# Kernel tuning notes

Measured on AMD Instinct MI355X. Metric: run time of the kernel, lower is better.

Reference implementation:

```python
import jax, jax.numpy as jnp
import numpy as np

OUT = 7   # output_size
SR = 2    # sampling_ratio


def _roi_align(feat, boxes, out_size, sr):
    """torchvision-style ROIAlign, spatial_scale=1.0, aligned=False.
    feat: [N,C,H,W], boxes: [K,5] (batch_idx,x1,y1,x2,y2) -> [K,C,out,out]."""
    N, C, H, W = feat.shape
    b = boxes[:, 0].astype(jnp.int32)                      # [K]
    x1, y1, x2, y2 = boxes[:, 1], boxes[:, 2], boxes[:, 3], boxes[:, 4]
    roi_w = jnp.maximum(x2 - x1, 1.0)
    roi_h = jnp.maximum(y2 - y1, 1.0)
    bin_h = roi_h / out_size
    bin_w = roi_w / out_size
    # sample offsets within each bin: (i + 0.5)/sr, i in [0,sr)
    off = (jnp.arange(sr, dtype=feat.dtype) + 0.5) / sr    # [sr]
    p = jnp.arange(out_size, dtype=feat.dtype)             # [out]
    # ys: [K, out*sr], xs: [K, out*sr]
    ys = (y1[:, None, None] + (p[None, :, None] + off[None, None, :]) * bin_h[:, None, None]).reshape(-1, out_size * sr)
    xs = (x1[:, None, None] + (p[None, :, None] + off[None, None, :]) * bin_w[:, None, None]).reshape(-1, out_size * sr)
    K = ys.shape[0]
    S = out_size * sr
    y = jnp.broadcast_to(ys[:, :, None], (K, S, S)).reshape(K, S * S)  # [K,P]
    x = jnp.broadcast_to(xs[:, None, :], (K, S, S)).reshape(K, S * S)
    valid = (y >= -1.0) & (y <= H) & (x >= -1.0) & (x <= W)
    y = jnp.clip(y, 0.0, H - 1)
    x = jnp.clip(x, 0.0, W - 1)
    y_lo = jnp.floor(y).astype(jnp.int32)
    x_lo = jnp.floor(x).astype(jnp.int32)
    y_hi = jnp.minimum(y_lo + 1, H - 1)
    x_hi = jnp.minimum(x_lo + 1, W - 1)
    ly = y - y_lo.astype(y.dtype)
    lx = x - x_lo.astype(x.dtype)
    hy = 1.0 - ly
    hx = 1.0 - lx
    feat_flat = feat.reshape(N, C, H * W)
    bb = b[:, None, None]                                   # [K,1,1]
    cc = jnp.arange(C)[None, :, None]                       # [1,C,1]

    def gather(yi, xi):
        idx = (yi * W + xi)[:, None, :]                     # [K,1,P]
        return feat_flat[bb, cc, idx]                       # [K,C,P]

    v = (gather(y_lo, x_lo) * (hy * hx)[:, None, :]
         + gather(y_lo, x_hi) * (hy * lx)[:, None, :]
         + gather(y_hi, x_lo) * (ly * hx)[:, None, :]
         + gather(y_hi, x_hi) * (ly * lx)[:, None, :])
    v = jnp.where(valid[:, None, :], v, 0.0)
    # average the sr*sr samples per bin
    v = v.reshape(K, C, out_size, sr, out_size, sr).mean(axis=(3, 5))
    return v


def setup_inputs() -> dict:
    key = jax.random.key(0)
    k1, k2, k3, k4, k5, k6 = jax.random.split(key, 6)
    N, C, H, W = 4, 256, 200, 200
    K = 512
    Hb = H // 2  # boxes live in the half-height band coord frame
    features = jax.random.normal(k1, (N, C, H, W), dtype=jnp.float32)
    b = jax.random.randint(k2, (K,), 0, N).astype(jnp.float32)
    cx = jax.random.uniform(k3, (K,)) * W
    cy = jax.random.uniform(k4, (K,)) * Hb
    bw = jax.random.uniform(k5, (K,)) * 60.0 + 8.0
    bh = jax.random.uniform(k6, (K,)) * 40.0 + 8.0
    x1 = jnp.clip(cx - bw / 2, 0.0, W - 2.0)
    x2 = jnp.clip(cx + bw / 2, x1 + 1.0, float(W))
    y1 = jnp.clip(cy - bh / 2, 0.0, Hb - 2.0)
    y2 = jnp.clip(cy + bh / 2, y1 + 1.0, float(Hb))
    boxes = jnp.stack([b, x1, y1, x2, y2], axis=1).astype(jnp.float32)
    return {"features": features, "boxes": boxes}


def reference(features, boxes):
    H = features.shape[2]
    feat_b1 = features[:, :, : H // 2, :]
    feat_b2 = features[:, :, H // 2 :, :]
    out_b1 = _roi_align(feat_b1, boxes, OUT, SR)
    out_b2 = _roi_align(feat_b2, boxes, OUT, SR)
    return jnp.concatenate([out_b1, out_b2], axis=1)  # [K, 2C, OUT, OUT]
```

## Files before the change

kernel.cpp:

```cpp
#include <hip/hip_runtime.h>

#define OUTSZ 7
#define SR 2
#define SS (OUTSZ*SR)
#define NS (SS*SS)
#define C_BAND 256
#define H_BAND 100
#define W_FULL 200
#define PLANE (2*H_BAND*W_FULL)
#define CCHUNK 64
#define NCHUNK (C_BAND/CCHUNK)
#define NBOX 512

__global__ __launch_bounds__(256) void sort_boxes_kernel(
    const float* __restrict__ boxes, int* __restrict__ perm)
{
    __shared__ int keys[NBOX];
    __shared__ int vals[NBOX];
    const int tid = threadIdx.x;
    for (int i = tid; i < NBOX; i += 256) {
        const int n = (int)boxes[i*5 + 0];
        const int y = (int)boxes[i*5 + 2];
        keys[i] = n * 256 + y;
        vals[i] = i;
    }
    __syncthreads();
    for (int size = 2; size <= NBOX; size <<= 1) {
        for (int stride = size >> 1; stride > 0; stride >>= 1) {
            const int i = (tid / stride) * (stride * 2) + (tid % stride);
            const int j = i + stride;
            const bool up = ((i & size) == 0);
            const int ki = keys[i], kj = keys[j];
            if ((ki > kj) == up) {
                keys[i] = kj; keys[j] = ki;
                const int v = vals[i]; vals[i] = vals[j]; vals[j] = v;
            }
            __syncthreads();
        }
    }
    for (int i = tid; i < NBOX; i += 256) perm[i] = vals[i];
}

__global__ __launch_bounds__(256) void roi_align_kernel(
    const float* __restrict__ feat,
    const float* __restrict__ boxes,
    const int*   __restrict__ perm,
    float* __restrict__ out)
{
    __shared__ int    s_i0[NS];
    __shared__ int    s_i1[NS];
    __shared__ float4 s_w[NS];

    const int b     = blockIdx.x;
    const int j     = b & 7;
    const int chunk = j & 3;
    const int band  = j >> 2;
    const int k     = perm[b >> 3];

    const int tid = threadIdx.x;

    const float bxf = boxes[k*5 + 0];
    const float x1  = boxes[k*5 + 1];
    const float y1  = boxes[k*5 + 2];
    const float x2  = boxes[k*5 + 3];
    const float y2  = boxes[k*5 + 4];
    const int   n   = (int)bxf;

    const float roi_w = fmaxf(x2 - x1, 1.0f);
    const float roi_h = fmaxf(y2 - y1, 1.0f);
    const float bin_w = roi_w / 7.0f;
    const float bin_h = roi_h / 7.0f;

    if (tid < NS) {
        const int sy = tid / SS;
        const int sx = tid - sy * SS;
        const int ph = sy >> 1, iy = sy & 1;
        const int pw = sx >> 1, ix = sx & 1;
        float y = y1 + ((float)ph + ((float)iy + 0.5f) * 0.5f) * bin_h;
        float x = x1 + ((float)pw + ((float)ix + 0.5f) * 0.5f) * bin_w;
        const bool valid = (y >= -1.0f) && (y <= (float)H_BAND) &&
                           (x >= -1.0f) && (x <= (float)W_FULL);
        y = fminf(fmaxf(y, 0.0f), (float)(H_BAND - 1));
        x = fminf(fmaxf(x, 0.0f), (float)(W_FULL - 1));
        const int y_lo = (int)floorf(y);
        const int x_lo = (int)floorf(x);
        const int y_hi = min(y_lo + 1, H_BAND - 1);
        const float ly = y - (float)y_lo;
        const float lx = x - (float)x_lo;
        const float hy = 1.0f - ly, hx = 1.0f - lx;
        const int xb = min(x_lo, W_FULL - 2);
        float w0, w1;
        if (x_lo == xb) { w0 = hx; w1 = lx; }
        else            { w0 = 0.0f; w1 = hx + lx; }
        const float vs = valid ? 1.0f : 0.0f;
        s_i0[tid] = y_lo * W_FULL + xb;
        s_i1[tid] = y_hi * W_FULL + xb;
        s_w[tid] = make_float4(hy * w0 * vs, hy * w1 * vs,
                               ly * w0 * vs, ly * w1 * vs);
    }
    __syncthreads();

    const int c0 = chunk * CCHUNK;
    const float* fbase = feat + (size_t)(n * C_BAND + c0) * PLANE
                              + (size_t)band * (H_BAND * W_FULL);
    float* obase = out + ((size_t)k * (2*C_BAND) + (size_t)band * C_BAND + c0)
                       * (OUTSZ * OUTSZ);

    const int NOUT = CCHUNK * OUTSZ * OUTSZ;
    for (int o = tid; o < NOUT; o += 256) {
        const int c   = o / 49;
        const int bin = o - c * 49;
        const int ph  = bin / 7;
        const int pw  = bin - ph * 7;
        const float* fc = fbase + (size_t)c * PLANE;
        const int s00 = (ph * 2) * SS + pw * 2;
        float acc = 0.0f;
        #pragma unroll
        for (int iy = 0; iy < 2; ++iy) {
            #pragma unroll
            for (int ix = 0; ix < 2; ++ix) {
                const int s = s00 + iy * SS + ix;
                const float4 w = s_w[s];
                const float2 a = *(const float2*)(fc + s_i0[s]);
                const float2 d = *(const float2*)(fc + s_i1[s]);
                acc += w.x * a.x + w.y * a.y + w.z * d.x + w.w * d.y;
            }
        }
        obase[o] = acc * 0.25f;
    }
}

extern "C" void kernel_launch(void* const* d_in, const int* in_sizes, int n_in,
                              void* d_out, int out_size, void* d_ws, size_t ws_size,
                              hipStream_t stream) {
    const float* feat  = (const float*)d_in[0];
    const float* boxes = (const float*)d_in[1];
    float* out = (float*)d_out;
    int* perm = (int*)d_ws;

    sort_boxes_kernel<<<1, 256, 0, stream>>>(boxes, perm);
    const int nblocks = NBOX * 2 * NCHUNK;
    roi_align_kernel<<<nblocks, 256, 0, stream>>>(feat, boxes, perm, out);
}
```

Baseline: 325.3 us.

## Stage ROI feature patches into LDS via global_load_lds before bilinear sampling

Instead of each thread gathering float2 pairs straight from global memory, each wavefront copies the ROI's bounding row/column patch for one channel into LDS with global_load_lds, and 196 threads then do the bilinear interpolation from LDS. Channels are processed four at a time per iteration, with two block barriers each time. The aim is coalesced patch loads and less redundant global gather traffic. In exchange it adds many barriers, leaves most threads idle during compute, holds up to 31 offsets per thread in registers, and needs large LDS, which may cut occupancy. It also loads the entire patch even when samples are sparse.

Result: slower. 332.7 us (+2.3%).

```diff
diff --git a/kernel.cpp b/kernel.cpp
--- a/kernel.cpp
+++ b/kernel.cpp
@@ -1,16 +1,22 @@
 #include <hip/hip_runtime.h>
 
 #define OUTSZ 7
-#define SR 2
-#define SS (OUTSZ*SR)
-#define NS (SS*SS)
+#define SS 14
+#define NS 196
 #define C_BAND 256
 #define H_BAND 100
 #define W_FULL 200
 #define PLANE (2*H_BAND*W_FULL)
 #define CCHUNK 64
-#define NCHUNK (C_BAND/CCHUNK)
 #define NBOX 512
+#define NC 4
+#define MAXROWS 28
+#define MAXSPANP 69
+#define PATCHF (MAXROWS*MAXSPANP)
+#define MAXI 31
+
+typedef const __attribute__((address_space(1))) void gvoid_t;
+typedef __attribute__((address_space(3))) void lvoid_t;
 
 __global__ __launch_bounds__(256) void sort_boxes_kernel(
     const float* __restrict__ boxes, int* __restrict__ perm)
@@ -47,17 +53,18 @@
     const int*   __restrict__ perm,
     float* __restrict__ out)
 {
-    __shared__ int    s_i0[NS];
-    __shared__ int    s_i1[NS];
+    __shared__ float  patch[NC][PATCHF];
     __shared__ float4 s_w[NS];
+    __shared__ int    s_o0[NS];
+    __shared__ int    s_o1[NS];
+    __shared__ int    rowy[MAXROWS];
 
     const int b     = blockIdx.x;
-    const int j     = b & 7;
-    const int chunk = j & 3;
-    const int band  = j >> 2;
+    const int jj    = b & 7;
+    const int chunk = jj & 3;
+    const int band  = jj >> 2;
     const int k     = perm[b >> 3];
-
-    const int tid = threadIdx.x;
+    const int tid   = threadIdx.x;
 
     const float bxf = boxes[k*5 + 0];
     const float x1  = boxes[k*5 + 1];
@@ -71,62 +78,118 @@
     const float bin_w = roi_w / 7.0f;
     const float bin_h = roi_h / 7.0f;
 
+    const float xA = fminf(fmaxf(x1 + 0.25f*bin_w, 0.f), 199.f);
+    const float xB = fminf(fmaxf(x1 + 6.75f*bin_w, 0.f), 199.f);
+    const int xoff  = min((int)floorf(xA), W_FULL - 2);
+    const int xbmax = min((int)floorf(xB), W_FULL - 2);
+    const int spanw  = xbmax - xoff + 2;
+    const int spanwP = spanw | 1;
+    const float yA = fminf(fmaxf(y1 + 0.25f*bin_h, 0.f), 99.f);
+    const float yB = fminf(fmaxf(y1 + 6.75f*bin_h, 0.f), 99.f);
+    const int rmin   = (int)floorf(yA);
+    const int rmaxr  = min((int)floorf(yB) + 1, H_BAND - 1);
+    const int contig = rmaxr - rmin + 1;
+    const bool layoutA = (contig <= MAXROWS);
+    const int nr = layoutA ? contig : MAXROWS;
+
     if (tid < NS) {
         const int sy = tid / SS;
         const int sx = tid - sy * SS;
-        const int ph = sy >> 1, iy = sy & 1;
-        const int pw = sx >> 1, ix = sx & 1;
-        float y = y1 + ((float)ph + ((float)iy + 0.5f) * 0.5f) * bin_h;
-        float x = x1 + ((float)pw + ((float)ix + 0.5f) * 0.5f) * bin_w;
-        const bool valid = (y >= -1.0f) && (y <= (float)H_BAND) &&
-                           (x >= -1.0f) && (x <= (float)W_FULL);
-        y = fminf(fmaxf(y, 0.0f), (float)(H_BAND - 1));
-        x = fminf(fmaxf(x, 0.0f), (float)(W_FULL - 1));
+        float y = y1 + ((float)(sy>>1) + ((float)(sy&1) + 0.5f) * 0.5f) * bin_h;
+        float x = x1 + ((float)(sx>>1) + ((float)(sx&1) + 0.5f) * 0.5f) * bin_w;
+        const bool valid = (y >= -1.0f) && (y <= 100.0f) &&
+                           (x >= -1.0f) && (x <= 200.0f);
+        y = fminf(fmaxf(y, 0.f), 99.f);
+        x = fminf(fmaxf(x, 0.f), 199.f);
         const int y_lo = (int)floorf(y);
         const int x_lo = (int)floorf(x);
         const int y_hi = min(y_lo + 1, H_BAND - 1);
         const float ly = y - (float)y_lo;
         const float lx = x - (float)x_lo;
-        const float hy = 1.0f - ly, hx = 1.0f - lx;
+        const float hy = 1.f - ly, hx = 1.f - lx;
         const int xb = min(x_lo, W_FULL - 2);
         float w0, w1;
-        if (x_lo == xb) { w0 = hx; w1 = lx; }
-        else            { w0 = 0.0f; w1 = hx + lx; }
-        const float vs = valid ? 1.0f : 0.0f;
-        s_i0[tid] = y_lo * W_FULL + xb;
-        s_i1[tid] = y_hi * W_FULL + xb;
-        s_w[tid] = make_float4(hy * w0 * vs, hy * w1 * vs,
-                               ly * w0 * vs, ly * w1 * vs);
-    }
+        if (x_lo == xb) { w0 = hx;  w1 = lx; }
+        else            { w0 = 0.f; w1 = hx + lx; }
+        const float vs = valid ? 1.f : 0.f;
+        const int xr = xb - xoff;
+        int rs0, rs1;
+        if (layoutA) { rs0 = y_lo - rmin; rs1 = y_hi - rmin; }
+        else         { rs0 = 2*sy;        rs1 = 2*sy + 1;    }
+        s_o0[tid] = rs0 * spanwP + xr;
+        s_o1[tid] = rs1 * spanwP + xr;
+        s_w[tid] = make_float4(hy*w0*vs, hy*w1*vs, ly*w0*vs, ly*w1*vs);
+        if (!layoutA && sx == 0) { rowy[2*sy] = y_lo; rowy[2*sy + 1] = y_hi; }
+    }
+    if (layoutA && tid < nr) rowy[tid] = rmin + tid;
     __syncthreads();
 
+    const int lane = tid & 63;
+    const int wv   = tid >> 6;
+    const int M  = nr * spanwP;
+    const int nI = (M + 63) >> 6;
+    int goff[MAXI];
+    #pragma unroll
+    for (int i = 0; i < MAXI; ++i) {
+        goff[i] = -1;
+        if (i < nI) {
+            const int slot = lane + (i << 6);
+            if (slot < M) {
+                const int r  = slot / spanwP;
+                const int xq = slot - r * spanwP;
+                if (xq < spanw)
+                    goff[i] = (rowy[r] * W_FULL + xoff + xq) * 4;
+            }
+        }
+    }
+
     const int c0 = chunk * CCHUNK;
-    const float* fbase = feat + (size_t)(n * C_BAND + c0) * PLANE
-                              + (size_t)band * (H_BAND * W_FULL);
-    float* obase = out + ((size_t)k * (2*C_BAND) + (size_t)band * C_BAND + c0)
-                       * (OUTSZ * OUTSZ);
-
-    const int NOUT = CCHUNK * OUTSZ * OUTSZ;
-    for (int o = tid; o < NOUT; o += 256) {
-        const int c   = o / 49;
-        const int bin = o - c * 49;
-        const int ph  = bin / 7;
-        const int pw  = bin - ph * 7;
-        const float* fc = fbase + (size_t)c * PLANE;
-        const int s00 = (ph * 2) * SS + pw * 2;
-        float acc = 0.0f;
+    const char* fb = (const char*)(feat + (size_t)(n * C_BAND + c0) * PLANE
+                                        + (size_t)band * (H_BAND * W_FULL));
+    float* ob = out + ((size_t)k * (2*C_BAND) + (size_t)band * C_BAND + c0)
+                    * (OUTSZ * OUTSZ);
+
+    const size_t cstride = (size_t)PLANE * 4;
+    const char* cb = fb + (size_t)wv * cstride;
+
+    for (int it = 0; it < CCHUNK / NC; ++it) {
         #pragma unroll
-        for (int iy = 0; iy < 2; ++iy) {
+        for (int i = 0; i < MAXI; ++i) {
+            if (i < nI) {
+                if (goff[i] >= 0) {
+                    __builtin_amdgcn_global_load_lds(
+                        (gvoid_t*)(cb + goff[i]),
+                        (lvoid_t*)(&patch[wv][i << 6]),
+                        4, 0, 0);
+                }
+            }
+        }
+        __syncthreads();
+
+        if (tid < NS) {
+            const int c_sub = tid / 49;
+            const int bin   = tid - c_sub * 49;
+            const int ph = bin / 7;
+            const int pw = bin - ph * 7;
+            const float* pb = &patch[c_sub][0];
+            const int s00 = (ph * 2) * SS + pw * 2;
+            float acc = 0.f;
             #pragma unroll
-            for (int ix = 0; ix < 2; ++ix) {
-                const int s = s00 + iy * SS + ix;
-                const float4 w = s_w[s];
-                const float2 a = *(const float2*)(fc + s_i0[s]);
-                const float2 d = *(const float2*)(fc + s_i1[s]);
-                acc += w.x * a.x + w.y * a.y + w.z * d.x + w.w * d.y;
-            }
-        }
-        obase[o] = acc * 0.25f;
+            for (int iy = 0; iy < 2; ++iy) {
+                #pragma unroll
+                for (int ix = 0; ix < 2; ++ix) {
+                    const int s = s00 + iy * SS + ix;
+                    const float4 w = s_w[s];
+                    const int o0 = s_o0[s];
+                    const int o1 = s_o1[s];
+                    acc += w.x * pb[o0] + w.y * pb[o0 + 1]
+                         + w.z * pb[o1] + w.w * pb[o1 + 1];
+                }
+            }
+            ob[(it * NC + c_sub) * 49 + bin] = acc * 0.25f;
+        }
+        __syncthreads();
+        cb += (size_t)NC * cstride;
     }
 }
 
@@ -139,6 +202,6 @@
     int* perm = (int*)d_ws;
 
     sort_boxes_kernel<<<1, 256, 0, stream>>>(boxes, perm);
-    const int nblocks = NBOX * 2 * NCHUNK;
+    const int nblocks = NBOX * 2 * 4;
     roi_align_kernel<<<nblocks, 256, 0, stream>>>(feat, boxes, perm, out);
 }
```

## Transpose features to channels-last and gather ROI samples with coalesced channel loads

Applied to the files above, without the earlier changes.

Adds a transpose kernel that writes the feature map to NHWC in workspace, then a gather kernel where each lane handles one channel, so every bilinear tap is a coalesced load across channels. Blocks are remapped so that units sharing an XCD process neighbouring sorted boxes, and results are staged through shared memory so the NCHW output is written coalesced. The cost is a full transpose of the whole 164MB feature map on every call, plus a larger workspace; a fallback to the old kernel remains for when the workspace is too small.

Result: slower. 358.2 us (+10.1%).

```diff
diff --git a/kernel.cpp b/kernel.cpp
--- a/kernel.cpp
+++ b/kernel.cpp
@@ -1,16 +1,15 @@
 #include <hip/hip_runtime.h>
 
 #define OUTSZ 7
-#define SR 2
-#define SS (OUTSZ*SR)
-#define NS (SS*SS)
+#define SS 14
+#define NS 196
 #define C_BAND 256
 #define H_BAND 100
+#define H_FULL 200
 #define W_FULL 200
-#define PLANE (2*H_BAND*W_FULL)
-#define CCHUNK 64
-#define NCHUNK (C_BAND/CCHUNK)
+#define POS (H_FULL*W_FULL)
 #define NBOX 512
+#define FEATT_OFF 4096
 
 __global__ __launch_bounds__(256) void sort_boxes_kernel(
     const float* __restrict__ boxes, int* __restrict__ perm)
@@ -41,23 +40,68 @@
     for (int i = tid; i < NBOX; i += 256) perm[i] = vals[i];
 }
 
-__global__ __launch_bounds__(256) void roi_align_kernel(
-    const float* __restrict__ feat,
+__global__ __launch_bounds__(256) void transpose_kernel(
+    const float* __restrict__ feat, float* __restrict__ featT)
+{
+    __shared__ float tile[64][65];
+    const int b    = blockIdx.x;
+    const int pt   = b % 625;
+    const int cg   = (b / 625) & 3;
+    const int n    = b / 2500;
+    const int c0   = cg * 64;
+    const int pos0 = pt * 64;
+    const int tid  = threadIdx.x;
+
+    {
+        const int xq = tid & 15;
+        const int cb = tid >> 4;
+        const float* src = feat + (size_t)(n * C_BAND + c0) * POS + pos0;
+        #pragma unroll
+        for (int r = 0; r < 4; ++r) {
+            const int ci = cb + (r << 4);
+            const float4 v = *(const float4*)(src + (size_t)ci * POS + (xq << 2));
+            tile[ci][(xq<<2)+0] = v.x;
+            tile[ci][(xq<<2)+1] = v.y;
+            tile[ci][(xq<<2)+2] = v.z;
+            tile[ci][(xq<<2)+3] = v.w;
+        }
+    }
+    __syncthreads();
+    {
+        const int cq = tid & 15;
+        const int pb = tid >> 4;
+        float* dst = featT + ((size_t)n * POS + pos0) * C_BAND + c0;
+        #pragma unroll
+        for (int r = 0; r < 4; ++r) {
+            const int pi = pb + (r << 4);
+            float4 v;
+            v.x = tile[(cq<<2)+0][pi];
+            v.y = tile[(cq<<2)+1][pi];
+            v.z = tile[(cq<<2)+2][pi];
+            v.w = tile[(cq<<2)+3][pi];
+            *(float4*)(dst + (size_t)pi * C_BAND + (cq<<2)) = v;
+        }
+    }
+}
+
+__global__ __launch_bounds__(256) void roi_gather_kernel(
+    const float* __restrict__ featT,
     const float* __restrict__ boxes,
     const int*   __restrict__ perm,
     float* __restrict__ out)
 {
-    __shared__ int    s_i0[NS];
-    __shared__ int    s_i1[NS];
+    __shared__ int    s_off[NS];
     __shared__ float4 s_w[NS];
-
-    const int b     = blockIdx.x;
-    const int j     = b & 7;
-    const int chunk = j & 3;
-    const int band  = j >> 2;
-    const int k     = perm[b >> 3];
-
-    const int tid = threadIdx.x;
+    __shared__ float  s_tile[4][64*49];
+
+    const int b    = blockIdx.x;
+    const int xcd  = b & 7;
+    const int unit = xcd * 128 + (b >> 3);
+    const int band = unit & 1;
+    const int k    = perm[unit >> 1];
+    const int tid  = threadIdx.x;
+    const int lane = tid & 63;
+    const int wv   = tid >> 6;
 
     const float bxf = boxes[k*5 + 0];
     const float x1  = boxes[k*5 + 1];
@@ -66,65 +110,129 @@
     const float y2  = boxes[k*5 + 4];
     const int   n   = (int)bxf;
 
-    const float roi_w = fmaxf(x2 - x1, 1.0f);
-    const float roi_h = fmaxf(y2 - y1, 1.0f);
-    const float bin_w = roi_w / 7.0f;
-    const float bin_h = roi_h / 7.0f;
+    const float bin_w = fmaxf(x2 - x1, 1.0f) * (1.0f / 7.0f);
+    const float bin_h = fmaxf(y2 - y1, 1.0f) * (1.0f / 7.0f);
 
     if (tid < NS) {
         const int sy = tid / SS;
         const int sx = tid - sy * SS;
-        const int ph = sy >> 1, iy = sy & 1;
-        const int pw = sx >> 1, ix = sx & 1;
-        float y = y1 + ((float)ph + ((float)iy + 0.5f) * 0.5f) * bin_h;
-        float x = x1 + ((float)pw + ((float)ix + 0.5f) * 0.5f) * bin_w;
-        const bool valid = (y >= -1.0f) && (y <= (float)H_BAND) &&
-                           (x >= -1.0f) && (x <= (float)W_FULL);
-        y = fminf(fmaxf(y, 0.0f), (float)(H_BAND - 1));
-        x = fminf(fmaxf(x, 0.0f), (float)(W_FULL - 1));
+        float y = y1 + ((float)(sy>>1) + ((float)(sy&1) + 0.5f) * 0.5f) * bin_h;
+        float x = x1 + ((float)(sx>>1) + ((float)(sx&1) + 0.5f) * 0.5f) * bin_w;
+        const bool valid = (y >= -1.0f) && (y <= 100.0f) &&
+                           (x >= -1.0f) && (x <= 200.0f);
+        y = fminf(fmaxf(y, 0.f), 99.f);
+        x = fminf(fmaxf(x, 0.f), 199.f);
         const int y_lo = (int)floorf(y);
         const int x_lo = (int)floorf(x);
-        const int y_hi = min(y_lo + 1, H_BAND - 1);
         const float ly = y - (float)y_lo;
         const float lx = x - (float)x_lo;
-        const float hy = 1.0f - ly, hx = 1.0f - lx;
+        const float hy = 1.f - ly, hx = 1.f - lx;
+        const int yb = min(y_lo, H_BAND - 2);
         const int xb = min(x_lo, W_FULL - 2);
-        float w0, w1;
-        if (x_lo == xb) { w0 = hx; w1 = lx; }
-        else            { w0 = 0.0f; w1 = hx + lx; }
-        const float vs = valid ? 1.0f : 0.0f;
-        s_i0[tid] = y_lo * W_FULL + xb;
-        s_i1[tid] = y_hi * W_FULL + xb;
-        s_w[tid] = make_float4(hy * w0 * vs, hy * w1 * vs,
-                               ly * w0 * vs, ly * w1 * vs);
-    }
-    __syncthreads();
-
-    const int c0 = chunk * CCHUNK;
-    const float* fbase = feat + (size_t)(n * C_BAND + c0) * PLANE
-                              + (size_t)band * (H_BAND * W_FULL);
-    float* obase = out + ((size_t)k * (2*C_BAND) + (size_t)band * C_BAND + c0)
-                       * (OUTSZ * OUTSZ);
-
-    const int NOUT = CCHUNK * OUTSZ * OUTSZ;
-    for (int o = tid; o < NOUT; o += 256) {
-        const int c   = o / 49;
-        const int bin = o - c * 49;
-        const int ph  = bin / 7;
-        const int pw  = bin - ph * 7;
-        const float* fc = fbase + (size_t)c * PLANE;
+        float wy0, wy1, wx0, wx1;
+        if (y_lo == yb) { wy0 = hy;  wy1 = ly; } else { wy0 = 0.f; wy1 = hy + ly; }
+        if (x_lo == xb) { wx0 = hx;  wx1 = lx; } else { wx0 = 0.f; wx1 = hx + lx; }
+        const float vs = valid ? 1.f : 0.f;
+        s_off[tid] = (((band * H_BAND + yb) * W_FULL) + xb) * (C_BAND * 4);
+        s_w[tid] = make_float4(wy0*wx0*vs, wy0*wx1*vs, wy1*wx0*vs, wy1*wx1*vs);
+    }
+    __syncthreads();
+
+    const char* base = (const char*)(featT + (size_t)n * POS * C_BAND
+                                           + (wv << 6) + lane);
+    const int ROWB = W_FULL * C_BAND * 4;
+
+    float* tl = s_tile[wv];
+    for (int bin = 0; bin < 49; ++bin) {
+        const int ph = bin / 7;
+        const int pw = bin - ph * 7;
         const int s00 = (ph * 2) * SS + pw * 2;
-        float acc = 0.0f;
+        float acc = 0.f;
         #pragma unroll
         for (int iy = 0; iy < 2; ++iy) {
             #pragma unroll
             for (int ix = 0; ix < 2; ++ix) {
                 const int s = s00 + iy * SS + ix;
                 const float4 w = s_w[s];
-                const float2 a = *(const float2*)(fc + s_i0[s]);
-                const float2 d = *(const float2*)(fc + s_i1[s]);
-                acc += w.x * a.x + w.y * a.y + w.z * d.x + w.w * d.y;
+                const char* p0 = base + s_off[s];
+                const char* p1 = p0 + ROWB;
+                const float v00 = *(const float*)(p0);
+                const float v01 = *(const float*)(p0 + C_BAND*4);
+                const float v10 = *(const float*)(p1);
+                const float v11 = *(const float*)(p1 + C_BAND*4);
+                acc += w.x*v00 + w.y*v01 + w.z*v10 + w.w*v11;
             }
+        }
+        tl[lane * 49 + bin] = acc * 0.25f;
+    }
+    __syncthreads();
+
+    float* dst = out + ((size_t)k * (2*C_BAND) + band * C_BAND + (wv << 6)) * 49;
+    #pragma unroll
+    for (int m = 0; m < 49; ++m) {
+        dst[(m << 6) + lane] = tl[(m << 6) + lane];
+    }
+}
+
+#define PLANE (2*H_BAND*W_FULL)
+#define CCHUNK 64
+__global__ __launch_bounds__(256) void roi_align_fallback(
+    const float* __restrict__ feat, const float* __restrict__ boxes,
+    const int* __restrict__ perm, float* __restrict__ out)
+{
+    __shared__ int    f_i0[NS];
+    __shared__ int    f_i1[NS];
+    __shared__ float4 f_w[NS];
+    const int b     = blockIdx.x;
+    const int jj    = b & 7;
+    const int chunk = jj & 3;
+    const int band  = jj >> 2;
+    const int k     = perm[b >> 3];
+    const int tid   = threadIdx.x;
+    const float bxf = boxes[k*5+0], x1 = boxes[k*5+1], y1 = boxes[k*5+2];
+    const float x2  = boxes[k*5+3], y2 = boxes[k*5+4];
+    const int   n   = (int)bxf;
+    const float bin_w = fmaxf(x2 - x1, 1.0f) * (1.0f/7.0f);
+    const float bin_h = fmaxf(y2 - y1, 1.0f) * (1.0f/7.0f);
+    if (tid < NS) {
+        const int sy = tid / SS, sx = tid - (tid / SS) * SS;
+        float y = y1 + ((float)(sy>>1) + ((float)(sy&1) + 0.5f) * 0.5f) * bin_h;
+        float x = x1 + ((float)(sx>>1) + ((float)(sx&1) + 0.5f) * 0.5f) * bin_w;
+        const bool valid = (y >= -1.f) && (y <= 100.f) && (x >= -1.f) && (x <= 200.f);
+        y = fminf(fmaxf(y, 0.f), 99.f);
+        x = fminf(fmaxf(x, 0.f), 199.f);
+        const int y_lo = (int)floorf(y), x_lo = (int)floorf(x);
+        const int y_hi = min(y_lo + 1, H_BAND - 1);
+        const float ly = y - (float)y_lo, lx = x - (float)x_lo;
+        const float hy = 1.f - ly, hx = 1.f - lx;
+        const int xb = min(x_lo, W_FULL - 2);
+        float w0, w1;
+        if (x_lo == xb) { w0 = hx; w1 = lx; } else { w0 = 0.f; w1 = hx + lx; }
+        const float vs = valid ? 1.f : 0.f;
+        f_i0[tid] = y_lo * W_FULL + xb;
+        f_i1[tid] = y_hi * W_FULL + xb;
+        f_w[tid] = make_float4(hy*w0*vs, hy*w1*vs, ly*w0*vs, ly*w1*vs);
+    }
+    __syncthreads();
+    const int c0 = chunk * CCHUNK;
+    const float* fbase = feat + (size_t)(n * C_BAND + c0) * PLANE
+                              + (size_t)band * (H_BAND * W_FULL);
+    float* obase = out + ((size_t)k * (2*C_BAND) + (size_t)band * C_BAND + c0) * 49;
+    for (int o = tid; o < CCHUNK * 49; o += 256) {
+        const int c = o / 49, bin = o - (o / 49) * 49;
+        const int ph = bin / 7, pw = bin - (bin / 7) * 7;
+        const float* fc = fbase + (size_t)c * PLANE;
+        const int s00 = (ph * 2) * SS + pw * 2;
+        float acc = 0.f;
+        #pragma unroll
+        for (int iy = 0; iy < 2; ++iy)
+        #pragma unroll
+        for (int ix = 0; ix < 2; ++ix) {
+            const int s = s00 + iy * SS + ix;
+            const float4 w = f_w[s];
+            const float2 a = *(const float2*)(fc + f_i0[s]);
+            const float2 d = *(const float2*)(fc + f_i1[s]);
+            acc += w.x * a.x + w.y * a.y + w.z * d.x + w.w * d.y;
         }
         obase[o] = acc * 0.25f;
     }
@@ -139,6 +247,13 @@
     int* perm = (int*)d_ws;
 
     sort_boxes_kernel<<<1, 256, 0, stream>>>(boxes, perm);
-    const int nblocks = NBOX * 2 * NCHUNK;
-    roi_align_kernel<<<nblocks, 256, 0, stream>>>(feat, boxes, perm, out);
-}
+
+    const size_t needT = FEATT_OFF + (size_t)4 * POS * C_BAND * sizeof(float);
+    if (ws_size >= needT) {
+        float* featT = (float*)((char*)d_ws + FEATT_OFF);
+        transpose_kernel<<<10000, 256, 0, stream>>>(feat, featT);
+        roi_gather_kernel<<<1024, 256, 0, stream>>>(featT, boxes, perm, out);
+    } else {
+        roi_align_fallback<<<NBOX * 8, 256, 0, stream>>>(feat, boxes, perm, out);
+    }
+}
```
